# Performance work log

Hardware: AMD Instinct MI355X
Metric: run time of the kernel (lower is better)

## Reference

```python
import jax, jax.numpy as jnp
import numpy as np

B = 2
H = W = 128
N = H * W            # 16384 nodes
K_LOC = 7 * 7        # 49 local neighbors (KxK unfold window)
K_LONG = int(K_LOC * 0.2)  # 9 long-range random neighbors
KT = K_LOC + K_LONG  # 58 total neighbors per node
D = 64               # prop_dim
EPS = 1e-12


def setup_inputs() -> dict:
    key = jax.random.key(0)
    k1, k2, k3 = jax.random.split(key, 3)
    logits = jax.random.normal(k1, (B, N, KT), dtype=jnp.float32)
    h0 = jax.random.normal(k2, (B, N, D), dtype=jnp.float32)
    v_inds = jax.random.randint(k3, (B, N, KT), 0, N)  # neighbor (column) indices
    return {"logits": logits, "h0": h0, "v_inds": v_inds, "num_iters": 10}


def reference(logits, h0, v_inds, num_iters):
    """Core of SymbolicGrouper.extract_segments:
    - local adjacency: softmax over K then max-normalize per row
    - scatter into (transposed) sparse global affinity: A[v, u] = adj[u, k], v = v_inds[u, k]
    - graph propagation: h <- normalize(A @ h), iterated.
    """
    Bn, Nn, Kt = logits.shape
    # local adjacency: softmax + max-normalize (matches extract_segments)
    adj = jax.nn.softmax(logits, axis=-1)
    adj = adj / jnp.clip(jnp.max(adj, axis=-1, keepdims=True), EPS, None)
    # validity mask (col_inds < N in local_to_sparse_global_affinity)
    adj = jnp.where(v_inds < Nn, adj, jnp.zeros((), adj.dtype))
    # h0 initialized as softmax of normal noise
    h = jax.nn.softmax(h0, axis=-1)

    def prop_one(adj_b, v_b, h_b):
        v_flat = v_b.reshape(-1)  # [N*K]

        def step(hc, _):
            # message from source node u along each of its K edges: [N, K, D]
            contrib = adj_b[:, :, None] * hc[:, None, :]
            # transposed scatter: accumulate into destination v (A^T semantics)
            out = jnp.zeros_like(hc).at[v_flat].add(contrib.reshape(-1, hc.shape[-1]))
            # per-node L2 renormalization keeps propagation stable
            out = out / jnp.clip(jnp.linalg.norm(out, axis=-1, keepdims=True), EPS, None)
            return out, None

        h_final, _ = jax.lax.scan(step, h_b, None, length=num_iters)
        return h_final

    return jax.vmap(prop_one)(adj, v_inds, h)  # [B, N, D]
```

## Files before the change

### kernel.cpp

```cpp
#include <hip/hip_runtime.h>
#include <hip/hip_fp16.h>

#define B_ 2
#define N_ 16384
#define KT_ 58
#define D_ 64
#define BN_ (B_ * N_)
#define EDGES_ (B_ * N_ * KT_)
#define NUM_ITERS_ 10
#define EPS_ 1e-12f
#define CAP_ 128
#define LCAP_ 112
#define NBIN_ 256
#define BINSZ_ 8192
#define P1BLK_ 256
#define P1CHUNK_ (EDGES_ / P1BLK_)

__global__ __launch_bounds__(256) void k_adj(const float* __restrict__ logits,
                                             const int* __restrict__ v_inds,
                                             unsigned int* __restrict__ packed) {
    const int lane = threadIdx.x & 63;
    const int r = blockIdx.x * 4 + (threadIdx.x >> 6);
    float l = (lane < KT_) ? logits[(size_t)r * KT_ + lane] : -INFINITY;
    float m = l;
    #pragma unroll
    for (int off = 32; off; off >>= 1) m = fmaxf(m, __shfl_xor(m, off));
    if (lane < KT_) {
        const int v = v_inds[(size_t)r * KT_ + lane];
        float w = (v < N_) ? __expf(l - m) : 0.f;
        unsigned int wb = (unsigned int)__half_as_ushort(__float2half_rn(w));
        unsigned int vv = (v < N_) ? (unsigned int)v : 0u;
        packed[(size_t)r * KT_ + lane] = (wb << 16) | vv;
    }
}

__global__ __launch_bounds__(256) void k_bin(const unsigned int* __restrict__ packed,
                                             int* __restrict__ gBinCnt,
                                             unsigned int* __restrict__ binRec,
                                             unsigned char* __restrict__ binRow) {
    __shared__ int cnt[NBIN_];
    __shared__ int base[NBIN_];
    __shared__ int cur[NBIN_];
    const int t = threadIdx.x;
    cnt[t] = 0;
    __syncthreads();
    const int e0 = blockIdx.x * P1CHUNK_;
    #pragma unroll 4
    for (int i = 0; i < P1CHUNK_ / 256; ++i) {
        const int e = e0 + i * 256 + t;
        const unsigned int pk = packed[e];
        const int gv = ((e >= N_ * KT_) ? N_ : 0) + (int)(pk & 0x3fffu);
        atomicAdd(&cnt[gv >> 7], 1);
    }
    __syncthreads();
    base[t] = atomicAdd(&gBinCnt[t], cnt[t]);
    cur[t] = 0;
    __syncthreads();
    #pragma unroll 4
    for (int i = 0; i < P1CHUNK_ / 256; ++i) {
        const int e = e0 + i * 256 + t;
        const unsigned int pk = packed[e];
        const int gv = ((e >= N_ * KT_) ? N_ : 0) + (int)(pk & 0x3fffu);
        const int bin = gv >> 7;
        const unsigned int u = (unsigned int)(e / KT_);
        const int slot = atomicAdd(&cur[bin], 1);
        const int pos = base[bin] + slot;
        if (pos < BINSZ_) {
            binRec[((size_t)bin << 13) + pos] = (pk & 0xffff0000u) | u;
            binRow[((size_t)bin << 13) + pos] = (unsigned char)(gv & 127);
        }
    }
}

__global__ __launch_bounds__(256) void k_bucket(const int* __restrict__ gBinCnt,
                                                const unsigned int* __restrict__ binRec,
                                                const unsigned char* __restrict__ binRow,
                                                unsigned int* __restrict__ bucket,
                                                int* __restrict__ dcnt) {
    __shared__ unsigned int rows[128 * LCAP_];
    __shared__ int rcnt[128];
    const int t = threadIdx.x;
    for (int i = t; i < 128 * LCAP_; i += 256) rows[i] = 0;
    if (t < 128) rcnt[t] = 0;
    __syncthreads();
    const int b = blockIdx.x;
    const int n = min(gBinCnt[b], BINSZ_);
    for (int i = t; i < n; i += 256) {
        const unsigned int rec = binRec[((size_t)b << 13) + i];
        const int row = (int)binRow[((size_t)b << 13) + i];
        const int slot = atomicAdd(&rcnt[row], 1);
        if (slot < LCAP_) rows[row * LCAP_ + slot] = rec;
    }
    __syncthreads();
    for (int i = t; i < 128 * CAP_; i += 256) {
        const int row = i >> 7, slot = i & 127;
        const unsigned int val = (slot < LCAP_) ? rows[row * LCAP_ + slot] : 0u;
        bucket[(((size_t)b << 7) + row) * CAP_ + slot] = val;
    }
    if (t < 128) dcnt[(b << 7) + t] = min(rcnt[t], LCAP_);
}

__global__ __launch_bounds__(256) void k_hinit(const float* __restrict__ h0,
                                               __half* __restrict__ h) {
    const int lane = threadIdx.x & 63;
    const int r = blockIdx.x * 4 + (threadIdx.x >> 6);
    float x = h0[(size_t)r * D_ + lane];
    float m = x;
    #pragma unroll
    for (int off = 32; off; off >>= 1) m = fmaxf(m, __shfl_xor(m, off));
    float ex = __expf(x - m);
    float s = ex;
    #pragma unroll
    for (int off = 32; off; off >>= 1) s += __shfl_xor(s, off);
    h[(size_t)r * D_ + lane] = __float2half_rn(ex / s);
}

#define FMA_MIX(ACC, PK, REC, SEL0)                                            \
    asm("v_fma_mix_f32 %0, %1, %2, %0 op_sel:[" SEL0 ",1,0] op_sel_hi:[1,1,0]" \
        : "+v"(ACC)                                                            \
        : "v"(PK), "v"(REC));

#define PROC_EDGE(REC, A0, A1, A2, A3, A4, A5, A6, A7)                        \
    {                                                                          \
        const int u = (int)((REC) & 0xffffu);                                  \
        const uint4 x = h4[(size_t)u * 8 + j];                                 \
        FMA_MIX(A0, x.x, (REC), "0")                                           \
        FMA_MIX(A1, x.x, (REC), "1")                                           \
        FMA_MIX(A2, x.y, (REC), "0")                                           \
        FMA_MIX(A3, x.y, (REC), "1")                                           \
        FMA_MIX(A4, x.z, (REC), "0")                                           \
        FMA_MIX(A5, x.z, (REC), "1")                                           \
        FMA_MIX(A6, x.w, (REC), "0")                                           \
        FMA_MIX(A7, x.w, (REC), "1")                                           \
    }

template <bool FINAL>
__global__ __launch_bounds__(256) void k_prop(const int* __restrict__ dcnt,
                                              const unsigned int* __restrict__ bucket,
                                              const __half* __restrict__ h_in,
                                              __half* __restrict__ h_out,
                                              float* __restrict__ out_f) {
    const int lane = threadIdx.x & 63;
    const int grp = lane >> 3;
    const int j = lane & 7;
    const int p = blockIdx.x & 7;
    const int m = blockIdx.x >> 3;
    const int wid = threadIdx.x >> 6;
    int g0 = (p << 12) + (((m << 2) + wid) << 1);
    g0 = __builtin_amdgcn_readfirstlane(g0);
    const int g1 = g0 + 1;

    const int cntA = dcnt[g0];
    const int cntB = dcnt[g1];
    const unsigned int* browA = bucket + (size_t)g0 * CAP_;
    const unsigned int* browB = bucket + (size_t)g1 * CAP_;
    const unsigned int r0A = browA[lane];
    const unsigned int r0B = browB[lane];
    const uint4* __restrict__ h4 = (const uint4*)h_in;

    float a0 = 0.f, a1 = 0.f, a2 = 0.f, a3 = 0.f;
    float a4 = 0.f, a5 = 0.f, a6 = 0.f, a7 = 0.f;
    float b0 = 0.f, b1 = 0.f, b2 = 0.f, b3 = 0.f;
    float b4 = 0.f, b5 = 0.f, b6 = 0.f, b7 = 0.f;

    #pragma unroll 4
    for (int e0 = 0; e0 < 64; e0 += 8) {
        const int e = e0 + grp;
        const unsigned int recA = __shfl(r0A, e);
        const unsigned int recB = __shfl(r0B, e);
        PROC_EDGE(recA, a0, a1, a2, a3, a4, a5, a6, a7)
        PROC_EDGE(recB, b0, b1, b2, b3, b4, b5, b6, b7)
    }
    if (cntA > 64) {
        const unsigned int r1A = browA[64 + lane];
        for (int e0 = 64; e0 < cntA; e0 += 8) {
            const int e = e0 + grp;
            unsigned int rec = __shfl(r1A, e & 63);
            rec = (e < cntA) ? rec : 0u;
            PROC_EDGE(rec, a0, a1, a2, a3, a4, a5, a6, a7)
        }
    }
    if (cntB > 64) {
        const unsigned int r1B = browB[64 + lane];
        for (int e0 = 64; e0 < cntB; e0 += 8) {
            const int e = e0 + grp;
            unsigned int rec = __shfl(r1B, e & 63);
            rec = (e < cntB) ? rec : 0u;
            PROC_EDGE(rec, b0, b1, b2, b3, b4, b5, b6, b7)
        }
    }

    #pragma unroll
    for (int off = 8; off <= 32; off <<= 1) {
        a0 += __shfl_xor(a0, off); a1 += __shfl_xor(a1, off);
        a2 += __shfl_xor(a2, off); a3 += __shfl_xor(a3, off);
        a4 += __shfl_xor(a4, off); a5 += __shfl_xor(a5, off);
        a6 += __shfl_xor(a6, off); a7 += __shfl_xor(a7, off);
        b0 += __shfl_xor(b0, off); b1 += __shfl_xor(b1, off);
        b2 += __shfl_xor(b2, off); b3 += __shfl_xor(b3, off);
        b4 += __shfl_xor(b4, off); b5 += __shfl_xor(b5, off);
        b6 += __shfl_xor(b6, off); b7 += __shfl_xor(b7, off);
    }

    float nA = a0 * a0 + a1 * a1 + a2 * a2 + a3 * a3 +
               a4 * a4 + a5 * a5 + a6 * a6 + a7 * a7;
    float nB = b0 * b0 + b1 * b1 + b2 * b2 + b3 * b3 +
               b4 * b4 + b5 * b5 + b6 * b6 + b7 * b7;
    #pragma unroll
    for (int off = 4; off; off >>= 1) {
        nA += __shfl_xor(nA, off);
        nB += __shfl_xor(nB, off);
    }
    const float invA = 1.0f / fmaxf(sqrtf(nA), EPS_);
    const float invB = 1.0f / fmaxf(sqrtf(nB), EPS_);

    if (grp == 0) {
        if (FINAL) {
            float4* oA = (float4*)out_f + (size_t)g0 * 16 + j * 2;
            oA[0] = make_float4(a0 * invA, a1 * invA, a2 * invA, a3 * invA);
            oA[1] = make_float4(a4 * invA, a5 * invA, a6 * invA, a7 * invA);
            float4* oB = (float4*)out_f + (size_t)g1 * 16 + j * 2;
            oB[0] = make_float4(b0 * invB, b1 * invB, b2 * invB, b3 * invB);
            oB[1] = make_float4(b4 * invB, b5 * invB, b6 * invB, b7 * invB);
        } else {
            __half2 q0 = __floats2half2_rn(a0 * invA, a1 * invA);
            __half2 q1 = __floats2half2_rn(a2 * invA, a3 * invA);
            __half2 q2 = __floats2half2_rn(a4 * invA, a5 * invA);
            __half2 q3 = __floats2half2_rn(a6 * invA, a7 * invA);
            uint4 oA;
            oA.x = *(const unsigned int*)&q0;
            oA.y = *(const unsigned int*)&q1;
            oA.z = *(const unsigned int*)&q2;
            oA.w = *(const unsigned int*)&q3;
            ((uint4*)h_out)[(size_t)g0 * 8 + j] = oA;
            __half2 s0 = __floats2half2_rn(b0 * invB, b1 * invB);
            __half2 s1 = __floats2half2_rn(b2 * invB, b3 * invB);
            __half2 s2 = __floats2half2_rn(b4 * invB, b5 * invB);
            __half2 s3 = __floats2half2_rn(b6 * invB, b7 * invB);
            uint4 oB;
            oB.x = *(const unsigned int*)&s0;
            oB.y = *(const unsigned int*)&s1;
            oB.z = *(const unsigned int*)&s2;
            oB.w = *(const unsigned int*)&s3;
            ((uint4*)h_out)[(size_t)g1 * 8 + j] = oB;
        }
    }
}

extern "C" void kernel_launch(void* const* d_in, const int* in_sizes, int n_in,
                              void* d_out, int out_size, void* d_ws, size_t ws_size,
                              hipStream_t stream) {
    const float* logits = (const float*)d_in[0];
    const float* h0 = (const float*)d_in[1];
    const int* v_inds = (const int*)d_in[2];
    float* out = (float*)d_out;

    char* ws = (char*)d_ws;
    size_t off = 0;
    auto alloc = [&](size_t bytes) {
        void* p = ws + off;
        off = (off + bytes + 255) & ~(size_t)255;
        return p;
    };
    unsigned int* bucket = (unsigned int*)alloc((size_t)BN_ * CAP_ * 4);
    unsigned int* packed = bucket;
    unsigned int* binRec = (unsigned int*)alloc((size_t)NBIN_ * BINSZ_ * 4);
    unsigned char* binRow = (unsigned char*)alloc((size_t)NBIN_ * BINSZ_);
    int* gBinCnt = (int*)alloc((size_t)NBIN_ * 4);
    int* dcnt    = (int*)alloc((size_t)BN_ * 4);
    __half* h_a  = (__half*)alloc((size_t)BN_ * D_ * 2);
    __half* h_b  = (__half*)alloc((size_t)BN_ * D_ * 2);

    hipMemsetAsync(gBinCnt, 0, (size_t)NBIN_ * 4, stream);

    k_adj<<<BN_ / 4, 256, 0, stream>>>(logits, v_inds, packed);
    k_hinit<<<BN_ / 4, 256, 0, stream>>>(h0, h_a);
    k_bin<<<P1BLK_, 256, 0, stream>>>(packed, gBinCnt, binRec, binRow);
    k_bucket<<<NBIN_, 256, 0, stream>>>(gBinCnt, binRec, binRow, bucket, dcnt);

    const __half* cur = h_a;
    for (int i = 0; i < NUM_ITERS_; ++i) {
        __half* nxt = (i & 1) ? h_a : h_b;
        if (i == NUM_ITERS_ - 1) {
            k_prop<true><<<BN_ / 8, 256, 0, stream>>>(dcnt, bucket, cur, nullptr, out);
        } else {
            k_prop<false><<<BN_ / 8, 256, 0, stream>>>(dcnt, bucket, cur, nxt, nullptr);
        }
        cur = nxt;
    }
}
```

Measured before the change: 345.6 us.

## Fuse adjacency and binning kernels; process four node pairs per wave in propagation

Merges the softmax-weight/packing kernel into the binning kernel, staging packed records in shared memory so the packed array is no longer written to and reread from global memory. Propagation now loops over four destination-node pairs per wave, launching a quarter as many blocks, and loads bucket records with nontemporal hints. This cuts kernel launches and intermediate traffic. The cost is lower block-level parallelism in propagation and more serial work per wave.

```diff
diff --git a/kernel.cpp b/kernel.cpp
--- a/kernel.cpp
+++ b/kernel.cpp
@@ -13,61 +13,55 @@
 #define LCAP_ 112
 #define NBIN_ 256
 #define BINSZ_ 8192
-#define P1BLK_ 256
-#define P1CHUNK_ (EDGES_ / P1BLK_)
-
-__global__ __launch_bounds__(256) void k_adj(const float* __restrict__ logits,
-                                             const int* __restrict__ v_inds,
-                                             unsigned int* __restrict__ packed) {
-    const int lane = threadIdx.x & 63;
-    const int r = blockIdx.x * 4 + (threadIdx.x >> 6);
-    float l = (lane < KT_) ? logits[(size_t)r * KT_ + lane] : -INFINITY;
-    float m = l;
-    #pragma unroll
-    for (int off = 32; off; off >>= 1) m = fmaxf(m, __shfl_xor(m, off));
-    if (lane < KT_) {
-        const int v = v_inds[(size_t)r * KT_ + lane];
-        float w = (v < N_) ? __expf(l - m) : 0.f;
-        unsigned int wb = (unsigned int)__half_as_ushort(__float2half_rn(w));
-        unsigned int vv = (v < N_) ? (unsigned int)v : 0u;
-        packed[(size_t)r * KT_ + lane] = (wb << 16) | vv;
-    }
-}
-
-__global__ __launch_bounds__(256) void k_bin(const unsigned int* __restrict__ packed,
-                                             int* __restrict__ gBinCnt,
-                                             unsigned int* __restrict__ binRec,
-                                             unsigned char* __restrict__ binRow) {
+#define ABROWS_ 32
+#define ABBLK_ (BN_ / ABROWS_)
+
+__global__ __launch_bounds__(256) void k_adjbin(const float* __restrict__ logits,
+                                                const int* __restrict__ v_inds,
+                                                int* __restrict__ gBinCnt,
+                                                unsigned int* __restrict__ binRec,
+                                                unsigned char* __restrict__ binRow) {
+    __shared__ unsigned int pkl[ABROWS_ * KT_];
     __shared__ int cnt[NBIN_];
     __shared__ int base[NBIN_];
     __shared__ int cur[NBIN_];
     const int t = threadIdx.x;
+    const int lane = t & 63;
+    const int wid = t >> 6;
     cnt[t] = 0;
     __syncthreads();
-    const int e0 = blockIdx.x * P1CHUNK_;
-    #pragma unroll 4
-    for (int i = 0; i < P1CHUNK_ / 256; ++i) {
-        const int e = e0 + i * 256 + t;
-        const unsigned int pk = packed[e];
-        const int gv = ((e >= N_ * KT_) ? N_ : 0) + (int)(pk & 0x3fffu);
-        atomicAdd(&cnt[gv >> 7], 1);
-    }
-    __syncthreads();
-    base[t] = atomicAdd(&gBinCnt[t], cnt[t]);
+    const int blk = blockIdx.x;
+    const int binOff = (blk >= ABBLK_ / 2) ? 128 : 0;
+    #pragma unroll
+    for (int it = 0; it < ABROWS_ / 4; ++it) {
+        const int rl = it * 4 + wid;
+        const int r = blk * ABROWS_ + rl;
+        float l = (lane < KT_) ? logits[(size_t)r * KT_ + lane] : -INFINITY;
+        float m = l;
+        #pragma unroll
+        for (int off = 32; off; off >>= 1) m = fmaxf(m, __shfl_xor(m, off));
+        if (lane < KT_) {
+            const int v = v_inds[(size_t)r * KT_ + lane];
+            float w = (v < N_) ? __expf(l - m) : 0.f;
+            unsigned int wb = (unsigned int)__half_as_ushort(__float2half_rn(w));
+            unsigned int vv = (v < N_) ? (unsigned int)v : 0u;
+            pkl[rl * KT_ + lane] = (wb << 16) | vv;
+            atomicAdd(&cnt[binOff + (int)(vv >> 7)], 1);
+        }
+    }
+    __syncthreads();
+    base[t] = cnt[t] ? atomicAdd(&gBinCnt[t], cnt[t]) : 0;
     cur[t] = 0;
     __syncthreads();
-    #pragma unroll 4
-    for (int i = 0; i < P1CHUNK_ / 256; ++i) {
-        const int e = e0 + i * 256 + t;
-        const unsigned int pk = packed[e];
-        const int gv = ((e >= N_ * KT_) ? N_ : 0) + (int)(pk & 0x3fffu);
-        const int bin = gv >> 7;
-        const unsigned int u = (unsigned int)(e / KT_);
+    for (int i = t; i < ABROWS_ * KT_; i += 256) {
+        const unsigned int pk = pkl[i];
+        const int bin = binOff + (int)((pk & 0x3fffu) >> 7);
+        const unsigned int u = (unsigned int)(blk * ABROWS_ + i / KT_);
         const int slot = atomicAdd(&cur[bin], 1);
         const int pos = base[bin] + slot;
         if (pos < BINSZ_) {
             binRec[((size_t)bin << 13) + pos] = (pk & 0xffff0000u) | u;
-            binRow[((size_t)bin << 13) + pos] = (unsigned char)(gv & 127);
+            binRow[((size_t)bin << 13) + pos] = (unsigned char)(pk & 127u);
         }
     }
 }
@@ -146,103 +140,107 @@
     const int p = blockIdx.x & 7;
     const int m = blockIdx.x >> 3;
     const int wid = threadIdx.x >> 6;
-    int g0 = (p << 12) + (((m << 2) + wid) << 1);
-    g0 = __builtin_amdgcn_readfirstlane(g0);
-    const int g1 = g0 + 1;
-
-    const int cntA = dcnt[g0];
-    const int cntB = dcnt[g1];
-    const unsigned int* browA = bucket + (size_t)g0 * CAP_;
-    const unsigned int* browB = bucket + (size_t)g1 * CAP_;
-    const unsigned int r0A = browA[lane];
-    const unsigned int r0B = browB[lane];
+    int gb = (p << 12) + ((m * 4 + wid) << 3);
+    gb = __builtin_amdgcn_readfirstlane(gb);
     const uint4* __restrict__ h4 = (const uint4*)h_in;
 
-    float a0 = 0.f, a1 = 0.f, a2 = 0.f, a3 = 0.f;
-    float a4 = 0.f, a5 = 0.f, a6 = 0.f, a7 = 0.f;
-    float b0 = 0.f, b1 = 0.f, b2 = 0.f, b3 = 0.f;
-    float b4 = 0.f, b5 = 0.f, b6 = 0.f, b7 = 0.f;
-
-    #pragma unroll 4
-    for (int e0 = 0; e0 < 64; e0 += 8) {
-        const int e = e0 + grp;
-        const unsigned int recA = __shfl(r0A, e);
-        const unsigned int recB = __shfl(r0B, e);
-        PROC_EDGE(recA, a0, a1, a2, a3, a4, a5, a6, a7)
-        PROC_EDGE(recB, b0, b1, b2, b3, b4, b5, b6, b7)
-    }
-    if (cntA > 64) {
-        const unsigned int r1A = browA[64 + lane];
-        for (int e0 = 64; e0 < cntA; e0 += 8) {
+    #pragma unroll 1
+    for (int pair = 0; pair < 4; ++pair) {
+        const int g0 = gb + pair * 2;
+        const int g1 = g0 + 1;
+        const int cntA = dcnt[g0];
+        const int cntB = dcnt[g1];
+        const unsigned int* browA = bucket + (size_t)g0 * CAP_;
+        const unsigned int* browB = bucket + (size_t)g1 * CAP_;
+        const unsigned int r0A = __builtin_nontemporal_load(browA + lane);
+        const unsigned int r0B = __builtin_nontemporal_load(browB + lane);
+
+        float a0 = 0.f, a1 = 0.f, a2 = 0.f, a3 = 0.f;
+        float a4 = 0.f, a5 = 0.f, a6 = 0.f, a7 = 0.f;
+        float b0 = 0.f, b1 = 0.f, b2 = 0.f, b3 = 0.f;
+        float b4 = 0.f, b5 = 0.f, b6 = 0.f, b7 = 0.f;
+
+        #pragma unroll 4
+        for (int e0 = 0; e0 < 64; e0 += 8) {
             const int e = e0 + grp;
-            unsigned int rec = __shfl(r1A, e & 63);
-            rec = (e < cntA) ? rec : 0u;
-            PROC_EDGE(rec, a0, a1, a2, a3, a4, a5, a6, a7)
-        }
-    }
-    if (cntB > 64) {
-        const unsigned int r1B = browB[64 + lane];
-        for (int e0 = 64; e0 < cntB; e0 += 8) {
-            const int e = e0 + grp;
-            unsigned int rec = __shfl(r1B, e & 63);
-            rec = (e < cntB) ? rec : 0u;
-            PROC_EDGE(rec, b0, b1, b2, b3, b4, b5, b6, b7)
-        }
-    }
-
-    #pragma unroll
-    for (int off = 8; off <= 32; off <<= 1) {
-        a0 += __shfl_xor(a0, off); a1 += __shfl_xor(a1, off);
-        a2 += __shfl_xor(a2, off); a3 += __shfl_xor(a3, off);
-        a4 += __shfl_xor(a4, off); a5 += __shfl_xor(a5, off);
-        a6 += __shfl_xor(a6, off); a7 += __shfl_xor(a7, off);
-        b0 += __shfl_xor(b0, off); b1 += __shfl_xor(b1, off);
-        b2 += __shfl_xor(b2, off); b3 += __shfl_xor(b3, off);
-        b4 += __shfl_xor(b4, off); b5 += __shfl_xor(b5, off);
-        b6 += __shfl_xor(b6, off); b7 += __shfl_xor(b7, off);
-    }
-
-    float nA = a0 * a0 + a1 * a1 + a2 * a2 + a3 * a3 +
-               a4 * a4 + a5 * a5 + a6 * a6 + a7 * a7;
-    float nB = b0 * b0 + b1 * b1 + b2 * b2 + b3 * b3 +
-               b4 * b4 + b5 * b5 + b6 * b6 + b7 * b7;
-    #pragma unroll
-    for (int off = 4; off; off >>= 1) {
-        nA += __shfl_xor(nA, off);
-        nB += __shfl_xor(nB, off);
-    }
-    const float invA = 1.0f / fmaxf(sqrtf(nA), EPS_);
-    const float invB = 1.0f / fmaxf(sqrtf(nB), EPS_);
-
-    if (grp == 0) {
-        if (FINAL) {
-            float4* oA = (float4*)out_f + (size_t)g0 * 16 + j * 2;
-            oA[0] = make_float4(a0 * invA, a1 * invA, a2 * invA, a3 * invA);
-            oA[1] = make_float4(a4 * invA, a5 * invA, a6 * invA, a7 * invA);
-            float4* oB = (float4*)out_f + (size_t)g1 * 16 + j * 2;
-            oB[0] = make_float4(b0 * invB, b1 * invB, b2 * invB, b3 * invB);
-            oB[1] = make_float4(b4 * invB, b5 * invB, b6 * invB, b7 * invB);
-        } else {
-            __half2 q0 = __floats2half2_rn(a0 * invA, a1 * invA);
-            __half2 q1 = __floats2half2_rn(a2 * invA, a3 * invA);
-            __half2 q2 = __floats2half2_rn(a4 * invA, a5 * invA);
-            __half2 q3 = __floats2half2_rn(a6 * invA, a7 * invA);
-            uint4 oA;
-            oA.x = *(const unsigned int*)&q0;
-            oA.y = *(const unsigned int*)&q1;
-            oA.z = *(const unsigned int*)&q2;
-            oA.w = *(const unsigned int*)&q3;
-            ((uint4*)h_out)[(size_t)g0 * 8 + j] = oA;
-            __half2 s0 = __floats2half2_rn(b0 * invB, b1 * invB);
-            __half2 s1 = __floats2half2_rn(b2 * invB, b3 * invB);
-            __half2 s2 = __floats2half2_rn(b4 * invB, b5 * invB);
-            __half2 s3 = __floats2half2_rn(b6 * invB, b7 * invB);
-            uint4 oB;
-            oB.x = *(const unsigned int*)&s0;
-            oB.y = *(const unsigned int*)&s1;
-            oB.z = *(const unsigned int*)&s2;
-            oB.w = *(const unsigned int*)&s3;
-            ((uint4*)h_out)[(size_t)g1 * 8 + j] = oB;
+            const unsigned int recA = __shfl(r0A, e);
+            const unsigned int recB = __shfl(r0B, e);
+            PROC_EDGE(recA, a0, a1, a2, a3, a4, a5, a6, a7)
+            PROC_EDGE(recB, b0, b1, b2, b3, b4, b5, b6, b7)
+        }
+        if (cntA > 64) {
+            const unsigned int r1A = __builtin_nontemporal_load(browA + 64 + lane);
+            for (int e0 = 64; e0 < cntA; e0 += 8) {
+                const int e = e0 + grp;
+                unsigned int rec = __shfl(r1A, e & 63);
+                rec = (e < cntA) ? rec : 0u;
+                PROC_EDGE(rec, a0, a1, a2, a3, a4, a5, a6, a7)
+            }
+        }
+        if (cntB > 64) {
+            const unsigned int r1B = __builtin_nontemporal_load(browB + 64 + lane);
+            for (int e0 = 64; e0 < cntB; e0 += 8) {
+                const int e = e0 + grp;
+                unsigned int rec = __shfl(r1B, e & 63);
+                rec = (e < cntB) ? rec : 0u;
+                PROC_EDGE(rec, b0, b1, b2, b3, b4, b5, b6, b7)
+            }
+        }
+
+        #pragma unroll
+        for (int off = 8; off <= 32; off <<= 1) {
+            a0 += __shfl_xor(a0, off); a1 += __shfl_xor(a1, off);
+            a2 += __shfl_xor(a2, off); a3 += __shfl_xor(a3, off);
+            a4 += __shfl_xor(a4, off); a5 += __shfl_xor(a5, off);
+            a6 += __shfl_xor(a6, off); a7 += __shfl_xor(a7, off);
+            b0 += __shfl_xor(b0, off); b1 += __shfl_xor(b1, off);
+            b2 += __shfl_xor(b2, off); b3 += __shfl_xor(b3, off);
+            b4 += __shfl_xor(b4, off); b5 += __shfl_xor(b5, off);
+            b6 += __shfl_xor(b6, off); b7 += __shfl_xor(b7, off);
+        }
+
+        float nA = a0 * a0 + a1 * a1 + a2 * a2 + a3 * a3 +
+                   a4 * a4 + a5 * a5 + a6 * a6 + a7 * a7;
+        float nB = b0 * b0 + b1 * b1 + b2 * b2 + b3 * b3 +
+                   b4 * b4 + b5 * b5 + b6 * b6 + b7 * b7;
+        #pragma unroll
+        for (int off = 4; off; off >>= 1) {
+            nA += __shfl_xor(nA, off);
+            nB += __shfl_xor(nB, off);
+        }
+        const float invA = 1.0f / fmaxf(sqrtf(nA), EPS_);
+        const float invB = 1.0f / fmaxf(sqrtf(nB), EPS_);
+
+        if (grp == 0) {
+            if (FINAL) {
+                float4* oA = (float4*)out_f + (size_t)g0 * 16 + j * 2;
+                oA[0] = make_float4(a0 * invA, a1 * invA, a2 * invA, a3 * invA);
+                oA[1] = make_float4(a4 * invA, a5 * invA, a6 * invA, a7 * invA);
+                float4* oB = (float4*)out_f + (size_t)g1 * 16 + j * 2;
+                oB[0] = make_float4(b0 * invB, b1 * invB, b2 * invB, b3 * invB);
+                oB[1] = make_float4(b4 * invB, b5 * invB, b6 * invB, b7 * invB);
+            } else {
+                __half2 q0 = __floats2half2_rn(a0 * invA, a1 * invA);
+                __half2 q1 = __floats2half2_rn(a2 * invA, a3 * invA);
+                __half2 q2 = __floats2half2_rn(a4 * invA, a5 * invA);
+                __half2 q3 = __floats2half2_rn(a6 * invA, a7 * invA);
+                uint4 oA;
+                oA.x = *(const unsigned int*)&q0;
+                oA.y = *(const unsigned int*)&q1;
+                oA.z = *(const unsigned int*)&q2;
+                oA.w = *(const unsigned int*)&q3;
+                ((uint4*)h_out)[(size_t)g0 * 8 + j] = oA;
+                __half2 s0 = __floats2half2_rn(b0 * invB, b1 * invB);
+                __half2 s1 = __floats2half2_rn(b2 * invB, b3 * invB);
+                __half2 s2 = __floats2half2_rn(b4 * invB, b5 * invB);
+                __half2 s3 = __floats2half2_rn(b6 * invB, b7 * invB);
+                uint4 oB;
+                oB.x = *(const unsigned int*)&s0;
+                oB.y = *(const unsigned int*)&s1;
+                oB.z = *(const unsigned int*)&s2;
+                oB.w = *(const unsigned int*)&s3;
+                ((uint4*)h_out)[(size_t)g1 * 8 + j] = oB;
+            }
         }
     }
 }
@@ -263,7 +261,6 @@
         return p;
     };
     unsigned int* bucket = (unsigned int*)alloc((size_t)BN_ * CAP_ * 4);
-    unsigned int* packed = bucket;
     unsigned int* binRec = (unsigned int*)alloc((size_t)NBIN_ * BINSZ_ * 4);
     unsigned char* binRow = (unsigned char*)alloc((size_t)NBIN_ * BINSZ_);
     int* gBinCnt = (int*)alloc((size_t)NBIN_ * 4);
@@ -273,18 +270,17 @@
 
     hipMemsetAsync(gBinCnt, 0, (size_t)NBIN_ * 4, stream);
 
-    k_adj<<<BN_ / 4, 256, 0, stream>>>(logits, v_inds, packed);
+    k_adjbin<<<ABBLK_, 256, 0, stream>>>(logits, v_inds, gBinCnt, binRec, binRow);
+    k_bucket<<<NBIN_, 256, 0, stream>>>(gBinCnt, binRec, binRow, bucket, dcnt);
     k_hinit<<<BN_ / 4, 256, 0, stream>>>(h0, h_a);
-    k_bin<<<P1BLK_, 256, 0, stream>>>(packed, gBinCnt, binRec, binRow);
-    k_bucket<<<NBIN_, 256, 0, stream>>>(gBinCnt, binRec, binRow, bucket, dcnt);
 
     const __half* cur = h_a;
     for (int i = 0; i < NUM_ITERS_; ++i) {
         __half* nxt = (i & 1) ? h_a : h_b;
         if (i == NUM_ITERS_ - 1) {
-            k_prop<true><<<BN_ / 8, 256, 0, stream>>>(dcnt, bucket, cur, nullptr, out);
+            k_prop<true><<<BN_ / 32, 256, 0, stream>>>(dcnt, bucket, cur, nullptr, out);
         } else {
-            k_prop<false><<<BN_ / 8, 256, 0, stream>>>(dcnt, bucket, cur, nxt, nullptr);
+            k_prop<false><<<BN_ / 32, 256, 0, stream>>>(dcnt, bucket, cur, nxt, nullptr);
         }
         cur = nxt;
     }
```

Measured after the change: 429.4 us. 1.24x slower.
